# Kernel tuning notes

Hardware: AMD Instinct MI355X
Metric: run time of the kernel (lower is better)

## Reference

```python
import jax, jax.numpy as jnp
import numpy as np

EPS = 1e-8

def _rasterize_mesh(face_verts, H, W):
    # face_verts: [F,3,3] = (ndc_x, ndc_y, view_z) per triangle vertex
    x0, y0, z0 = face_verts[:, 0, 0], face_verts[:, 0, 1], face_verts[:, 0, 2]
    x1, y1, z1 = face_verts[:, 1, 0], face_verts[:, 1, 1], face_verts[:, 1, 2]
    x2, y2, z2 = face_verts[:, 2, 0], face_verts[:, 2, 1], face_verts[:, 2, 2]
    area = (x1 - x0) * (y2 - y0) - (y1 - y0) * (x2 - x0)
    # cull_backfaces=True (area<=0) + degenerate + behind-camera cull
    face_ok = (area > EPS) & (z0 > 0) & (z1 > 0) & (z2 > 0)
    inv_area = jnp.where(face_ok, 1.0 / jnp.where(face_ok, area, 1.0), 0.0)
    zs = jnp.stack([z0, z1, z2], -1)  # [F,3]
    # pytorch3d NDC: +x left, +y up, pixel centers
    xs = 1.0 - (2.0 * jnp.arange(W, dtype=jnp.float32) + 1.0) / W
    ys = 1.0 - (2.0 * jnp.arange(H, dtype=jnp.float32) + 1.0) / H

    def row_fn(py):
        px = xs[:, None]  # [W,1] broadcast vs faces [F]
        w0 = ((x1 - px) * (y2 - py) - (y1 - py) * (x2 - px)) * inv_area
        w1 = ((x2 - px) * (y0 - py) - (y2 - py) * (x0 - px)) * inv_area
        w2 = ((x0 - px) * (y1 - py) - (y0 - py) * (x1 - px)) * inv_area
        inside = (w0 >= 0) & (w1 >= 0) & (w2 >= 0) & face_ok
        # perspective_correct=True: l_i = w_i * prod(other z), renormalize
        l = jnp.stack([w0 * z1 * z2, z0 * w1 * z2, z0 * z1 * w2], -1)  # [W,F,3]
        s = l.sum(-1, keepdims=True)
        b = l / jnp.where(s == 0, 1.0, s)
        # clip_barycentric_coords=True
        b = jnp.clip(b, 0.0, None)
        b = b / jnp.clip(b.sum(-1, keepdims=True), EPS, None)
        zpix = (b * zs[None]).sum(-1)  # [W,F] interpolated view-space depth
        zm = jnp.where(inside, zpix, jnp.inf)
        fidx = jnp.argmin(zm, axis=1)  # z-buffer winner per pixel
        zmin = jnp.take_along_axis(zm, fidx[:, None], 1)[:, 0]
        hit = jnp.isfinite(zmin)
        bary = jnp.take_along_axis(b, fidx[:, None, None], 1)[:, 0]  # [W,3]
        return (jnp.where(hit, fidx, -1),
                jnp.where(hit, zmin, -1.0),
                jnp.where(hit[:, None], bary, -1.0))

    return jax.lax.map(row_fn, ys)  # ([H,W],[H,W],[H,W,3])


def _forward(positions, features, faces, K, RT, H, W):
    B, V, _ = positions.shape
    Fn = faces.shape[1]
    # --- create_camera_objects: open3d/opencv KRT -> pytorch3d camera ---
    R = RT[:, :, :3]
    t = RT[:, :, 3]
    scale = min(H, W) / 2.0
    focal = jnp.stack([K[:, 0, 0], K[:, 1, 1]], -1) / scale  # [B,2] NDC focal
    p0 = -(jnp.stack([K[:, 0, 2], K[:, 1, 2]], -1)
           - jnp.array([W / 2.0, H / 2.0], jnp.float32)) / scale  # [B,2]
    sign = jnp.array([-1.0, -1.0, 1.0], jnp.float32)
    R_p = jnp.swapaxes(R, 1, 2) * sign[None, None, :]  # R^T with cols 0,1 negated
    T_p = t * sign[None, :]
    # --- _get_mesh_ndc: world -> view -> NDC (pytorch3d row-vector convention) ---
    v_view = jnp.einsum('bvi,bij->bvj', positions, R_p) + T_p[:, None, :]
    z = v_view[..., 2:3]
    xy_ndc = focal[:, None, :] * v_view[..., :2] / z + p0[:, None, :]
    verts_ndc = jnp.concatenate([xy_ndc, z], -1)  # z overwritten with view-space depth
    face_verts = jax.vmap(lambda v, f: v[f])(verts_ndc, faces)  # [B,F,3,3]
    # --- rasterize (blur_sigma=0 -> faces_per_pixel=1) ---
    p2f, zbuf, bary = jax.vmap(lambda fv: _rasterize_mesh(fv, H, W))(face_verts)
    hit = p2f >= 0
    pix_to_face = jnp.where(hit, p2f + (jnp.arange(B) * Fn)[:, None, None], -1)
    # --- interpolate_face_attributes on packed faces/verts ---
    faces_packed = (faces + (jnp.arange(B) * V)[:, None, None]).reshape(B * Fn, 3)
    feats_packed = features.reshape(B * V, -1)
    fv_idx = faces_packed[jnp.clip(pix_to_face, 0)]  # [B,H,W,3]
    attrs = feats_packed[fv_idx]                      # [B,H,W,3,C]
    pix_feats = (bary[..., None] * attrs).sum(-2)
    pix_feats = jnp.where(hit[..., None], pix_feats, 0.0)
    dists = jnp.where(hit, 0.0, -1.0)
    # add faces_per_pixel (K=1) axis, matching pytorch3d Fragments layout
    return (pix_feats[:, :, :, None, :], pix_to_face[:, :, :, None],
            zbuf[:, :, :, None], bary[:, :, :, None, :], dists[:, :, :, None])


def setup_inputs() -> dict:
    key = jax.random.key(0)
    k1, k2, k3 = jax.random.split(key, 3)
    B, V, Fn, C, H, W = 1, 8192, 16384, 64, 192, 192
    positions = jax.random.uniform(k1, (B, V, 3), jnp.float32) * 2.0 - 1.0
    features = jax.random.normal(k2, (B, V, C), jnp.float32)
    faces = jax.random.randint(k3, (B, Fn, 3), 0, V)
    K = jnp.broadcast_to(jnp.array([[180.0, 0.0, 96.0], [0.0, 180.0, 96.0],
                                    [0.0, 0.0, 1.0]], jnp.float32), (B, 3, 3))
    RT = jnp.broadcast_to(jnp.concatenate(
        [jnp.eye(3, dtype=jnp.float32),
         jnp.array([[0.0], [0.0], [3.5]], jnp.float32)], axis=1), (B, 3, 4))
    return {"positions": positions, "features": features, "faces": faces,
            "K": K, "RT": RT, "H": H, "W": W, "blur_sigma": 0}


def reference(positions, features, faces, K, RT, H, W, blur_sigma):
    # blur_sigma == 0 path of VertexShader.forward (faces_per_pixel=1)
    return _forward(positions, features, faces, K, RT, H, W)
```

## Files before the change

### kernel.cpp

```cpp
#include <hip/hip_runtime.h>
#include <stdint.h>

#define H_ 192
#define W_ 192
#define C_ 64
#define EPS_F 1e-8f
#define TILE 16
#define NTX (W_/TILE)
#define NTY (H_/TILE)
#define CHUNK 256
#define NSLICE 8
#define NBUCKET 256
#define MAXCHUNK 64

typedef unsigned long long ull;

#define OFF_FEATS 0
#define OFF_P2F   (H_*W_*C_)
#define OFF_ZBUF  (OFF_P2F + H_*W_)
#define OFF_BARY  (OFF_ZBUF + H_*W_)
#define OFF_DIST  (OFF_BARY + H_*W_*3)

__device__ __forceinline__ float xm(float a, float b){ return __fmul_rn(a,b); }
__device__ __forceinline__ float xa(float a, float b){ return __fadd_rn(a,b); }
__device__ __forceinline__ float xsb(float a, float b){ return __fsub_rn(a,b); }
__device__ __forceinline__ float xd(float a, float b){ return __fdiv_rn(a,b); }

__device__ __forceinline__ float pixcoord(int i, float dim){
    float t = xa(xm(2.0f, (float)i), 1.0f);
    return xsb(1.0f, xd(t, dim));
}

__device__ __forceinline__ unsigned fenc(float f){
    unsigned b = __float_as_uint(f);
    return (b & 0x80000000u) ? ~b : (b | 0x80000000u);
}
__device__ __forceinline__ float fdec(unsigned e){
    unsigned b = (e & 0x80000000u) ? (e & 0x7FFFFFFFu) : ~e;
    return __uint_as_float(b);
}

__device__ __forceinline__ int zbucket(float zmn){
    int b = (int)((zmn - 2.0f) * 64.0f);
    return b < 0 ? 0 : (b > 254 ? 254 : b);
}
__device__ __forceinline__ float zlo_bucket(int b){
    if (b >= 255) return INFINITY;
    if (b == 0)   return 0.0f;
    return 2.0f + (float)b * 0.015625f;
}

__device__ __forceinline__ float3 tv(const float* __restrict__ pos,
        const float* __restrict__ K, const float* __restrict__ RT, int i){
    float p0 = pos[3*i+0], p1 = pos[3*i+1], p2 = pos[3*i+2];
    const float sgn[3] = {-1.f, -1.f, 1.f};
    float vv[3];
    #pragma unroll
    for (int j=0;j<3;j++){
        float rp0 = xm(RT[j*4+0], sgn[j]);
        float rp1 = xm(RT[j*4+1], sgn[j]);
        float rp2 = xm(RT[j*4+2], sgn[j]);
        float s = xa(xa(xm(p0,rp0), xm(p1,rp1)), xm(p2,rp2));
        vv[j] = xa(s, xm(RT[j*4+3], sgn[j]));
    }
    float z = vv[2];
    float fx = xd(K[0], 96.0f);
    float fy = xd(K[4], 96.0f);
    float p0x = -xd(xsb(K[2], 96.0f), 96.0f);
    float p0y = -xd(xsb(K[5], 96.0f), 96.0f);
    float xn = xa(xd(xm(fx, vv[0]), z), p0x);
    float yn = xa(xd(xm(fy, vv[1]), z), p0y);
    return make_float3(xn, yn, z);
}

__global__ __launch_bounds__(64) void k_pre(const float* __restrict__ pos,
        const float* __restrict__ K, const float* __restrict__ RT,
        const int* __restrict__ faces, float* __restrict__ rec0,
        unsigned* __restrict__ hist, unsigned* __restrict__ gbb,
        ull* __restrict__ keys, int Fn){
    __shared__ unsigned lh[NBUCKET];
    int t = threadIdx.x, B = blockIdx.x;
    int gthreads = gridDim.x*64;
    for (int i = B*64 + t; i < H_*W_; i += gthreads) keys[i] = 0xFFFFFFFFFFFFFFFFULL;
    #pragma unroll
    for (int i=t; i<NBUCKET; i+=64) lh[i] = 0u;
    __syncthreads();
    int f = B*64 + t;
    float bxmn=INFINITY, bxmx=-INFINITY, bymn=INFINITY, bymx=-INFINITY;
    if (f < Fn){
        int i0 = faces[3*f+0], i1 = faces[3*f+1], i2 = faces[3*f+2];
        float3 v0 = tv(pos,K,RT,i0), v1 = tv(pos,K,RT,i1), v2 = tv(pos,K,RT,i2);
        float area = xsb(xm(xsb(v1.x,v0.x), xsb(v2.y,v0.y)), xm(xsb(v1.y,v0.y), xsb(v2.x,v0.x)));
        bool ok = (area > EPS_F) && (v0.z > 0.f) && (v1.z > 0.f) && (v2.z > 0.f);
        float ia = ok ? xd(1.0f, area) : 0.0f;
        float zmn = INFINITY;
        int b = 255;
        if (ok){
            zmn = fminf(v0.z, fminf(v1.z, v2.z));
            b = zbucket(zmn);
            bxmn = fminf(v0.x, fminf(v1.x, v2.x)) - 1e-4f;
            bxmx = fmaxf(v0.x, fmaxf(v1.x, v2.x)) + 1e-4f;
            bymn = fminf(v0.y, fminf(v1.y, v2.y)) - 1e-4f;
            bymx = fmaxf(v0.y, fmaxf(v1.y, v2.y)) + 1e-4f;
        }
        atomicAdd(&lh[b], 1u);
        float4* q = (float4*)(rec0 + (size_t)f*12);
        q[0] = make_float4(v0.x, v0.y, v1.x, v1.y);
        q[1] = make_float4(v2.x, v2.y, v0.z, v1.z);
        q[2] = make_float4(v2.z, ia, __int_as_float(f), zmn);
    }
    #pragma unroll
    for (int s2=1; s2<64; s2<<=1){
        bxmn = fminf(bxmn, __shfl_xor(bxmn, s2, 64));
        bxmx = fmaxf(bxmx, __shfl_xor(bxmx, s2, 64));
        bymn = fminf(bymn, __shfl_xor(bymn, s2, 64));
        bymx = fmaxf(bymx, __shfl_xor(bymx, s2, 64));
    }
    if (t == 0 && bxmx > -INFINITY){
        atomicMax(&gbb[0], fenc(-bxmn));
        atomicMax(&gbb[1], fenc( bxmx));
        atomicMax(&gbb[2], fenc(-bymn));
        atomicMax(&gbb[3], fenc( bymx));
    }
    __syncthreads();
    #pragma unroll
    for (int i=t; i<NBUCKET; i+=64){
        unsigned cc = lh[i];
        if (cc) atomicAdd(&hist[i], cc);
    }
}

__global__ __launch_bounds__(256) void k_scatter(const float* __restrict__ rec0,
        const unsigned* __restrict__ hist, unsigned* __restrict__ histcur,
        float* __restrict__ rec, float* __restrict__ suffz, int Fn){
    __shared__ unsigned gst[NBUCKET], ssc[NBUCKET], lcnt[NBUCKET], lbase[NBUCKET];
    int t = threadIdx.x, B = blockIdx.x;
    unsigned hv = hist[t];
    ssc[t] = hv;
    lcnt[t] = 0u;
    __syncthreads();
    for (int d=1; d<NBUCKET; d<<=1){
        unsigned u = (t >= d) ? ssc[t-d] : 0u;
        __syncthreads();
        ssc[t] += u;
        __syncthreads();
    }
    gst[t] = ssc[t] - hv;
    __syncthreads();
    if (B == 0 && t < MAXCHUNK){
        unsigned pos = (unsigned)t * CHUNK;
        int bb = 0;
        #pragma unroll
        for (int s = 128; s > 0; s >>= 1){
            int nb = bb + s;
            if (nb <= NBUCKET && ssc[nb-1] <= pos) bb = nb;
        }
        suffz[t] = zlo_bucket(bb);
    }
    int f = B*256 + t;
    bool valid = (f < Fn);
    float4 q0, q1, q2;
    int b = 255; unsigned rank = 0; bool ok = false; float zmn = INFINITY;
    if (valid){
        const float4* q = (const float4*)(rec0 + (size_t)f*12);
        q0 = q[0]; q1 = q[1]; q2 = q[2];
        ok = (q2.y > 0.f);
        zmn = q2.w;
        b = ok ? zbucket(zmn) : 255;
        rank = atomicAdd(&lcnt[b], 1u);
    }
    __syncthreads();
    unsigned add = lcnt[t];
    if (add) lbase[t] = atomicAdd(&histcur[t], add);
    __syncthreads();
    if (valid){
        float x0=q0.x, y0=q0.y, x1=q0.z, y1=q0.w;
        float x2=q1.x, y2=q1.y, z0=q1.z, z1=q1.w;
        float z2=q2.x, ia=q2.y;
        float xmn, xmx, ymn, ymx, Ap=0.f, Bp=0.f, Cp=0.f;
        if (ok){
            xmn = fminf(x0, fminf(x1, x2)) - 1e-4f;
            xmx = fmaxf(x0, fmaxf(x1, x2)) + 1e-4f;
            ymn = fminf(y0, fminf(y1, y2)) - 1e-4f;
            ymx = fmaxf(y0, fmaxf(y1, y2)) + 1e-4f;
            float iz0 = 1.f/z0, iz1 = 1.f/z1, iz2 = 1.f/z2;
            Ap = ia * ((y1-y2)*iz0 + (y2-y0)*iz1 + (y0-y1)*iz2);
            Bp = ia * ((x2-x1)*iz0 + (x0-x2)*iz1 + (x1-x0)*iz2);
            Cp = ia * ((x1*y2-x2*y1)*iz0 + (x2*y0-x0*y2)*iz1 + (x0*y1-x1*y0)*iz2);
        } else {
            xmn = INFINITY; xmx = -INFINITY; ymn = INFINITY; ymx = -INFINITY;
        }
        unsigned p = gst[b] + lbase[b] + rank;
        float4* qo = (float4*)(rec + (size_t)p*20);
        qo[0] = q0; qo[1] = q1; qo[2] = q2;
        qo[3] = make_float4(Ap, Bp, Cp, 0.f);
        qo[4] = make_float4(xmn, xmx, ymn, ymx);
    }
}

__global__ __launch_bounds__(256) void k_raster(const float* __restrict__ rec,
        const float* __restrict__ suffz, const unsigned* __restrict__ gbb,
        ull* __restrict__ keys, int Fn){
    __shared__ float lds[CHUNK*12];
    __shared__ float zl[CHUNK];
    __shared__ float pA[CHUNK], pB[CHUNK], pC[CHUNK], pM[CHUNK];
    __shared__ int   slist[CHUNK];
    __shared__ int   wcnt[4];
    __shared__ float suff[MAXCHUNK];
    int tid = threadIdx.x;
    int nchunk = (Fn + CHUNK - 1) / CHUNK;
    if (tid < MAXCHUNK) suff[tid] = suffz[tid];
    int ix = blockIdx.x*TILE + (tid & 15);
    int iy = blockIdx.y*TILE + (tid >> 4);
    int pix = iy*W_ + ix;
    float px = pixcoord(ix, (float)W_);
    float py = pixcoord(iy, (float)H_);
    float tx_hi = pixcoord(blockIdx.x*TILE,          (float)W_);
    float tx_lo = pixcoord(blockIdx.x*TILE + TILE-1, (float)W_);
    float ty_hi = pixcoord(blockIdx.y*TILE,          (float)H_);
    float ty_lo = pixcoord(blockIdx.y*TILE + TILE-1, (float)H_);
    float axmax = fmaxf(fabsf(tx_lo), fabsf(tx_hi));
    float bymax = fmaxf(fabsf(ty_lo), fabsf(ty_hi));
    float gx0 = -fdec(gbb[0]), gx1 = fdec(gbb[1]);
    float gy0 = -fdec(gbb[2]), gy1 = fdec(gbb[3]);
    bool alive = (px >= gx0) && (px <= gx1) && (py >= gy0) && (py <= gy1);
    int lane = tid & 63, wv = tid >> 6;
    float py_hi_w = pixcoord(blockIdx.y*TILE + wv*4,     (float)H_);
    float py_lo_w = pixcoord(blockIdx.y*TILE + wv*4 + 3, (float)H_);

    float zcut = alive ? INFINITY : -INFINITY;
    ull localkey = 0xFFFFFFFFFFFFFFFFULL;
    ull published = 0xFFFFFFFFFFFFFFFFULL;
    __syncthreads();

    int c = (int)blockIdx.z;
    float4 r0, r1, r2, r3, r4;
    r0 = r1 = r2 = r3 = r4 = make_float4(0,0,0,0);
    if (c < nchunk){
        int fi = c*CHUNK + tid;
        if (fi < Fn){
            const float4* gq = (const float4*)(rec + (size_t)fi*20);
            r0 = gq[0]; r1 = gq[1]; r2 = gq[2]; r3 = gq[3]; r4 = gq[4];
        }
    }

    while (c < nchunk){
        ull g = __hip_atomic_load(&keys[pix], __ATOMIC_RELAXED, __HIP_MEMORY_SCOPE_AGENT);
        float zg = __uint_as_float((unsigned)(g >> 32));
        zcut = fminf(zcut, zg);
        float sc = (c < MAXCHUNK) ? suff[c] : 0.0f;
        int done = (!alive || !(xm(sc, 0.999f) < zcut)) ? 1 : 0;
        if (__syncthreads_and(done)) break;

        int fi = c*CHUNK + tid;
        bool keep = false;
        float zb = 0.f, Ap = 0.f, Bp = 0.f, Cp = 0.f, Me = 0.f;
        if (fi < Fn){
            keep = (r4.x <= tx_hi) && (r4.y >= tx_lo) && (r4.z <= ty_hi) && (r4.w >= ty_lo);
            if (keep){
                Ap = r3.x; Bp = r3.y; Cp = r3.z;
                Me = 1e-5f*(fabsf(Ap)*axmax + fabsf(Bp)*bymax + fabsf(Cp)) + 1e-30f;
                float ax = (Ap > 0.f) ? tx_hi : tx_lo;
                float by = (Bp > 0.f) ? ty_hi : ty_lo;
                float Nub = Cp + Ap*ax + Bp*by + Me;
                if (!(Nub > 0.f)) keep = false;
                else zb = fmaxf(1.f/Nub, r2.w);
            }
        }
        float4* l = (float4*)(lds + tid*12);
        l[0] = r0; l[1] = r1; l[2] = r2;
        ull m = __ballot(keep);
        if (lane == 0) wcnt[wv] = __popcll(m);
        __syncthreads();
        int basecnt = 0;
        #pragma unroll
        for (int w2 = 0; w2 < 4; ++w2) if (w2 < wv) basecnt += wcnt[w2];
        if (keep){
            int p = basecnt + __popcll(m & ((1ULL << lane) - 1ULL));
            slist[p] = tid;
            zl[p] = zb;
            pA[p] = Ap; pB[p] = Bp; pC[p] = Cp; pM[p] = Me;
        }
        int nsurv = wcnt[0] + wcnt[1] + wcnt[2] + wcnt[3];
        __syncthreads();

        int cn = c + NSLICE;
        if (cn < nchunk){
            int fj = cn*CHUNK + tid;
            if (fj < Fn){
                const float4* gq = (const float4*)(rec + (size_t)fj*20);
                r0 = gq[0]; r1 = gq[1]; r2 = gq[2]; r3 = gq[3]; r4 = gq[4];
            }
        }

        float zcmax = zcut;
        #pragma unroll
        for (int s2=1; s2<64; s2<<=1) zcmax = fmaxf(zcmax, __shfl_xor(zcmax, s2, 64));

        for (int k0 = 0; k0 < nsurv; k0 += 64){
            int kk = k0 + lane;
            bool maybe = false;
            if (kk < nsurv){
                float A = pA[kk], Bc = pB[kk], Cc = pC[kk];
                float ax = (A  > 0.f) ? tx_hi  : tx_lo;
                float by = (Bc > 0.f) ? py_hi_w : py_lo_w;
                float Nub = Cc + A*ax + Bc*by + pM[kk];
                bool skip_plane = !(Nub > 0.f) || !(zcmax*Nub > 0.999f);
                bool skip_zl = !(xm(zl[kk], 0.999f) < zcmax);
                maybe = !skip_plane && !skip_zl;
            }
            ull wm = __ballot(maybe);
            while (wm){
                int k = (int)__ffsll(wm) - 1;
                wm &= wm - 1;
                k += k0;
                if (!(xm(zl[k], 0.999f) < zcut)) continue;
                float A = pA[k], Bc = pB[k], Cc = pC[k];
                float Nub = Cc + A*px + Bc*py + pM[k];
                if (!(Nub > 0.f)) continue;
                if (!(zcut*Nub > 0.999f)) continue;
                int j = slist[k];
                const float* r = lds + j*12;
                float x0=r[0], y0=r[1], x1=r[2], y1=r[3], x2=r[4], y2=r[5];
                float dx0=xsb(x0,px), dx1=xsb(x1,px), dx2=xsb(x2,px);
                float dy0=xsb(y0,py), dy1=xsb(y1,py), dy2=xsb(y2,py);
                float e0 = xsb(xm(dx1,dy2), xm(dy1,dx2));
                float e1 = xsb(xm(dx2,dy0), xm(dy2,dx0));
                float e2 = xsb(xm(dx0,dy1), xm(dy0,dx1));
                if (e0 >= 0.f && e1 >= 0.f && e2 >= 0.f){
                    float z0=r[6], z1=r[7], z2=r[8], ia=r[9];
                    float w0 = xm(e0, ia), w1 = xm(e1, ia), w2 = xm(e2, ia);
                    float l0 = xm(xm(w0,z1),z2);
                    float l1 = xm(xm(z0,w1),z2);
                    float l2 = xm(xm(z0,z1),w2);
                    float s  = xa(xa(l0,l1),l2);
                    float dn = (s == 0.f) ? 1.0f : s;
                    float b0 = fmaxf(xd(l0,dn), 0.f);
                    float b1 = fmaxf(xd(l1,dn), 0.f);
                    float b2 = fmaxf(xd(l2,dn), 0.f);
                    float bs = fmaxf(xa(xa(b0,b1),b2), EPS_F);
                    b0 = xd(b0,bs); b1 = xd(b1,bs); b2 = xd(b2,bs);
                    float zp = xa(xa(xm(b0,z0),xm(b1,z1)),xm(b2,z2));
                    ull ck = (((ull)__float_as_uint(zp)) << 32) | (unsigned)__float_as_int(r[10]);
                    if (ck < localkey) localkey = ck;
                    zcut = fminf(zcut, zp);
                }
            }
        }
        if (localkey < published){
            atomicMin(&keys[pix], localkey);
            published = localkey;
        }
        c = cn;
    }
    if (localkey < published) atomicMin(&keys[pix], localkey);
}

__global__ __launch_bounds__(256) void k_post(const ull* __restrict__ keys,
        const float* __restrict__ rec0, const float* __restrict__ feats,
        const int* __restrict__ faces, float* __restrict__ out){
    int grp = threadIdx.x >> 6;
    int c = threadIdx.x & 63;
    int pix = blockIdx.x*4 + grp;
    float* p2f  = out + OFF_P2F;
    float* zbuf = out + OFF_ZBUF;
    float* bary = out + OFF_BARY;
    float* dist = out + OFF_DIST;
    ull key = keys[pix];
    if (key == 0xFFFFFFFFFFFFFFFFULL){
        out[OFF_FEATS + pix*C_ + c] = 0.0f;
        if (c == 0){
            p2f[pix] = -1.0f; zbuf[pix] = -1.0f; dist[pix] = -1.0f;
        }
        if (c < 3) bary[3*pix+c] = -1.0f;
        return;
    }
    int f = (int)(key & 0xFFFFFFFFu);
    float z = __uint_as_float((unsigned)(key >> 32));
    int ix = pix % W_, iy = pix / W_;
    float px = pixcoord(ix, (float)W_);
    float py = pixcoord(iy, (float)H_);
    const float4* q = (const float4*)(rec0 + (size_t)f*12);
    float4 q0 = q[0], q1 = q[1], q2 = q[2];
    float x0=q0.x, y0=q0.y, x1=q0.z, y1=q0.w;
    float x2=q1.x, y2=q1.y, z0=q1.z, z1=q1.w;
    float z2=q2.x, ia=q2.y;
    float w0 = xm(xsb(xm(xsb(x1,px),xsb(y2,py)), xm(xsb(y1,py),xsb(x2,px))), ia);
    float w1 = xm(xsb(xm(xsb(x2,px),xsb(y0,py)), xm(xsb(y2,py),xsb(x0,px))), ia);
    float w2 = xm(xsb(xm(xsb(x0,px),xsb(y1,py)), xm(xsb(y0,py),xsb(x1,px))), ia);
    float l0 = xm(xm(w0,z1),z2);
    float l1 = xm(xm(z0,w1),z2);
    float l2 = xm(xm(z0,z1),w2);
    float s  = xa(xa(l0,l1),l2);
    float dn = (s == 0.f) ? 1.0f : s;
    float b0 = fmaxf(xd(l0,dn), 0.f);
    float b1 = fmaxf(xd(l1,dn), 0.f);
    float b2 = fmaxf(xd(l2,dn), 0.f);
    float bs = fmaxf(xa(xa(b0,b1),b2), EPS_F);
    b0 = xd(b0,bs); b1 = xd(b1,bs); b2 = xd(b2,bs);
    int i0 = faces[3*f+0], i1 = faces[3*f+1], i2 = faces[3*f+2];
    float res = xa(xa(xm(b0, feats[i0*C_ + c]), xm(b1, feats[i1*C_ + c])),
                   xm(b2, feats[i2*C_ + c]));
    out[OFF_FEATS + pix*C_ + c] = res;
    if (c == 0){
        p2f[pix] = (float)f; zbuf[pix] = z; dist[pix] = 0.0f;
    }
    if (c < 3){
        float bb = (c == 0) ? b0 : ((c == 1) ? b1 : b2);
        bary[3*pix+c] = bb;
    }
}

extern "C" void kernel_launch(void* const* d_in, const int* in_sizes, int n_in,
                              void* d_out, int out_size, void* d_ws, size_t ws_size,
                              hipStream_t stream) {
    const float* positions = (const float*)d_in[0];
    const float* features  = (const float*)d_in[1];
    const int*   faces     = (const int*)  d_in[2];
    const float* K         = (const float*)d_in[3];
    const float* RT        = (const float*)d_in[4];
    int Fn = in_sizes[2] / 3;

    ull*      keys     = (ull*)d_ws;
    unsigned* hist     = (unsigned*)(keys + H_*W_);
    unsigned* histcur  = hist + NBUCKET;
    unsigned* gbb      = histcur + NBUCKET;
    float*    suffz    = (float*)(gbb + 4);
    float*    rec      = suffz + MAXCHUNK;
    float*    rec0     = rec + (size_t)Fn*20;

    size_t regB = (NBUCKET*2 + 4)*4;
    hipMemsetAsync(hist, 0x00, regB, stream);

    int nfb = (Fn + 255) / 256;
    k_pre<<<(Fn+63)/64, 64, 0, stream>>>(positions, K, RT, faces, rec0, hist, gbb, keys, Fn);
    k_scatter<<<nfb, 256, 0, stream>>>(rec0, hist, histcur, rec, suffz, Fn);
    dim3 rg(NTX, NTY, NSLICE);
    k_raster<<<rg, dim3(256,1,1), 0, stream>>>(rec, suffz, gbb, keys, Fn);
    k_post<<<(H_*W_)/4, 256, 0, stream>>>(keys, rec0, features, faces, (float*)d_out);
}
```

Baseline: 144.1 us.

## Replace global histogram atomics and memset with per-block slabs and prefix reduction

k_pre now writes each block's bucket histogram and bounding box to per-block slabs instead of doing global atomicAdd/atomicMax. k_scatter sums the slabs itself to get global totals and per-block prefix offsets, which gives a deterministic scatter order. This removes the hipMemsetAsync launch and the global atomics on histcur. In exchange, every scatter block reads npre*256 slab entries (256 rows), a redundant serial loop that may cost more than the atomics it replaces.

```diff
diff --git a/kernel.cpp b/kernel.cpp
--- a/kernel.cpp
+++ b/kernel.cpp
@@ -29,15 +29,6 @@
 __device__ __forceinline__ float pixcoord(int i, float dim){
     float t = xa(xm(2.0f, (float)i), 1.0f);
     return xsb(1.0f, xd(t, dim));
-}
-
-__device__ __forceinline__ unsigned fenc(float f){
-    unsigned b = __float_as_uint(f);
-    return (b & 0x80000000u) ? ~b : (b | 0x80000000u);
-}
-__device__ __forceinline__ float fdec(unsigned e){
-    unsigned b = (e & 0x80000000u) ? (e & 0x7FFFFFFFu) : ~e;
-    return __uint_as_float(b);
 }
 
 __device__ __forceinline__ int zbucket(float zmn){
@@ -76,7 +67,7 @@
 __global__ __launch_bounds__(64) void k_pre(const float* __restrict__ pos,
         const float* __restrict__ K, const float* __restrict__ RT,
         const int* __restrict__ faces, float* __restrict__ rec0,
-        unsigned* __restrict__ hist, unsigned* __restrict__ gbb,
+        unsigned* __restrict__ slab, float* __restrict__ slabb,
         ull* __restrict__ keys, int Fn){
     __shared__ unsigned lh[NBUCKET];
     int t = threadIdx.x, B = blockIdx.x;
@@ -116,27 +107,30 @@
         bymn = fminf(bymn, __shfl_xor(bymn, s2, 64));
         bymx = fmaxf(bymx, __shfl_xor(bymx, s2, 64));
     }
-    if (t == 0 && bxmx > -INFINITY){
-        atomicMax(&gbb[0], fenc(-bxmn));
-        atomicMax(&gbb[1], fenc( bxmx));
-        atomicMax(&gbb[2], fenc(-bymn));
-        atomicMax(&gbb[3], fenc( bymx));
+    if (t == 0){
+        slabb[B*4+0] = bxmn; slabb[B*4+1] = bxmx;
+        slabb[B*4+2] = bymn; slabb[B*4+3] = bymx;
     }
     __syncthreads();
     #pragma unroll
-    for (int i=t; i<NBUCKET; i+=64){
-        unsigned cc = lh[i];
-        if (cc) atomicAdd(&hist[i], cc);
-    }
+    for (int i=t; i<NBUCKET; i+=64) slab[B*NBUCKET + i] = lh[i];
 }
 
 __global__ __launch_bounds__(256) void k_scatter(const float* __restrict__ rec0,
-        const unsigned* __restrict__ hist, unsigned* __restrict__ histcur,
-        float* __restrict__ rec, float* __restrict__ suffz, int Fn){
-    __shared__ unsigned gst[NBUCKET], ssc[NBUCKET], lcnt[NBUCKET], lbase[NBUCKET];
+        const unsigned* __restrict__ slab, const float* __restrict__ slabb,
+        float* __restrict__ gbbf, float* __restrict__ rec,
+        float* __restrict__ suffz, int Fn, int npre){
+    __shared__ unsigned gst[NBUCKET], ssc[NBUCKET], cpre[NBUCKET], lcnt[NBUCKET];
     int t = threadIdx.x, B = blockIdx.x;
-    unsigned hv = hist[t];
-    ssc[t] = hv;
+    unsigned pre = 0, tot = 0;
+    int rlim = 4*B;
+    for (int r2 = 0; r2 < npre; r2++){
+        unsigned v = slab[r2*NBUCKET + t];
+        tot += v;
+        if (r2 < rlim) pre += v;
+    }
+    cpre[t] = pre;
+    ssc[t] = tot;
     lcnt[t] = 0u;
     __syncthreads();
     for (int d=1; d<NBUCKET; d<<=1){
@@ -145,17 +139,32 @@
         ssc[t] += u;
         __syncthreads();
     }
-    gst[t] = ssc[t] - hv;
-    __syncthreads();
-    if (B == 0 && t < MAXCHUNK){
-        unsigned pos = (unsigned)t * CHUNK;
-        int bb = 0;
+    gst[t] = ssc[t] - tot;
+    __syncthreads();
+    if (B == 0){
+        if (t < MAXCHUNK){
+            unsigned pos = (unsigned)t * CHUNK;
+            int bb = 0;
+            #pragma unroll
+            for (int s = 128; s > 0; s >>= 1){
+                int nb = bb + s;
+                if (nb <= NBUCKET && ssc[nb-1] <= pos) bb = nb;
+            }
+            suffz[t] = zlo_bucket(bb);
+        }
+        int w = t >> 6, lanel = t & 63;
+        bool ismin = (w == 0) || (w == 2);
+        float v = ismin ? INFINITY : -INFINITY;
+        for (int r2 = lanel; r2 < npre; r2 += 64){
+            float u = slabb[r2*4 + w];
+            v = ismin ? fminf(v, u) : fmaxf(v, u);
+        }
         #pragma unroll
-        for (int s = 128; s > 0; s >>= 1){
-            int nb = bb + s;
-            if (nb <= NBUCKET && ssc[nb-1] <= pos) bb = nb;
-        }
-        suffz[t] = zlo_bucket(bb);
+        for (int s2=1; s2<64; s2<<=1){
+            float o = __shfl_xor(v, s2, 64);
+            v = ismin ? fminf(v, o) : fmaxf(v, o);
+        }
+        if (lanel == 0) gbbf[w] = v;
     }
     int f = B*256 + t;
     bool valid = (f < Fn);
@@ -169,9 +178,6 @@
         b = ok ? zbucket(zmn) : 255;
         rank = atomicAdd(&lcnt[b], 1u);
     }
-    __syncthreads();
-    unsigned add = lcnt[t];
-    if (add) lbase[t] = atomicAdd(&histcur[t], add);
     __syncthreads();
     if (valid){
         float x0=q0.x, y0=q0.y, x1=q0.z, y1=q0.w;
@@ -190,7 +196,7 @@
         } else {
             xmn = INFINITY; xmx = -INFINITY; ymn = INFINITY; ymx = -INFINITY;
         }
-        unsigned p = gst[b] + lbase[b] + rank;
+        unsigned p = gst[b] + cpre[b] + rank;
         float4* qo = (float4*)(rec + (size_t)p*20);
         qo[0] = q0; qo[1] = q1; qo[2] = q2;
         qo[3] = make_float4(Ap, Bp, Cp, 0.f);
@@ -199,7 +205,7 @@
 }
 
 __global__ __launch_bounds__(256) void k_raster(const float* __restrict__ rec,
-        const float* __restrict__ suffz, const unsigned* __restrict__ gbb,
+        const float* __restrict__ suffz, const float* __restrict__ gbbf,
         ull* __restrict__ keys, int Fn){
     __shared__ float lds[CHUNK*12];
     __shared__ float zl[CHUNK];
@@ -221,8 +227,8 @@
     float ty_lo = pixcoord(blockIdx.y*TILE + TILE-1, (float)H_);
     float axmax = fmaxf(fabsf(tx_lo), fabsf(tx_hi));
     float bymax = fmaxf(fabsf(ty_lo), fabsf(ty_hi));
-    float gx0 = -fdec(gbb[0]), gx1 = fdec(gbb[1]);
-    float gy0 = -fdec(gbb[2]), gy1 = fdec(gbb[3]);
+    float gx0 = gbbf[0], gx1 = gbbf[1];
+    float gy0 = gbbf[2], gy1 = gbbf[3];
     bool alive = (px >= gx0) && (px <= gx1) && (py >= gy0) && (py <= gy1);
     int lane = tid & 63, wv = tid >> 6;
     float py_hi_w = pixcoord(blockIdx.y*TILE + wv*4,     (float)H_);
@@ -420,22 +426,20 @@
     const float* K         = (const float*)d_in[3];
     const float* RT        = (const float*)d_in[4];
     int Fn = in_sizes[2] / 3;
-
-    ull*      keys     = (ull*)d_ws;
-    unsigned* hist     = (unsigned*)(keys + H_*W_);
-    unsigned* histcur  = hist + NBUCKET;
-    unsigned* gbb      = histcur + NBUCKET;
-    float*    suffz    = (float*)(gbb + 4);
-    float*    rec      = suffz + MAXCHUNK;
-    float*    rec0     = rec + (size_t)Fn*20;
-
-    size_t regB = (NBUCKET*2 + 4)*4;
-    hipMemsetAsync(hist, 0x00, regB, stream);
-
-    int nfb = (Fn + 255) / 256;
-    k_pre<<<(Fn+63)/64, 64, 0, stream>>>(positions, K, RT, faces, rec0, hist, gbb, keys, Fn);
-    k_scatter<<<nfb, 256, 0, stream>>>(rec0, hist, histcur, rec, suffz, Fn);
+    int npre = (Fn + 63) / 64;
+    int nsc  = (Fn + 255) / 256;
+
+    ull*      keys  = (ull*)d_ws;
+    unsigned* slab  = (unsigned*)(keys + H_*W_);
+    float*    slabb = (float*)(slab + (size_t)npre*NBUCKET);
+    float*    gbbf  = slabb + (size_t)npre*4;
+    float*    suffz = gbbf + 4;
+    float*    rec   = suffz + MAXCHUNK;
+    float*    rec0  = rec + (size_t)Fn*20;
+
+    k_pre<<<npre, 64, 0, stream>>>(positions, K, RT, faces, rec0, slab, slabb, keys, Fn);
+    k_scatter<<<nsc, 256, 0, stream>>>(rec0, slab, slabb, gbbf, rec, suffz, Fn, npre);
     dim3 rg(NTX, NTY, NSLICE);
-    k_raster<<<rg, dim3(256,1,1), 0, stream>>>(rec, suffz, gbb, keys, Fn);
+    k_raster<<<rg, dim3(256,1,1), 0, stream>>>(rec, suffz, gbbf, keys, Fn);
     k_post<<<(H_*W_)/4, 256, 0, stream>>>(keys, rec0, features, faces, (float*)d_out);
 }
```

Result: slower. 163.8 us (+13.7%).
